# Performance work log

Measured on AMD Instinct MI355X. Metric: run time of the kernel, lower is better.

## Reference

```python
import jax, jax.numpy as jnp
import numpy as np

NUM_INPUTS = 512
NUM_OUTPUTS = 256
NUM_NODES = 20000
NUM_EDGES = 640000
NUM_LAYERS = 6
BATCH = 128


def setup_inputs() -> dict:
    rng = np.random.default_rng(0)
    chunk = (NUM_NODES - NUM_INPUTS) // NUM_LAYERS  # 3248 nodes per topo layer
    # destination node of each edge: any non-input node
    dst = rng.integers(NUM_INPUTS, NUM_INPUTS + chunk * NUM_LAYERS, NUM_EDGES)
    layer_of = (dst - NUM_INPUTS) // chunk
    layer_start = NUM_INPUTS + layer_of * chunk  # first node index of dst's layer
    # source strictly in an earlier layer (or an input node) -> layered DAG
    src = (rng.random(NUM_EDGES) * layer_start).astype(np.int64)
    act_id = rng.integers(0, 3, NUM_NODES)  # 0=sigmoid, 1=tanh, 2=relu
    layer_masks = np.zeros((NUM_LAYERS, NUM_NODES), dtype=bool)
    for l in range(NUM_LAYERS):
        layer_masks[l, NUM_INPUTS + l * chunk: NUM_INPUTS + (l + 1) * chunk] = True
    key = jax.random.key(0)
    kx, kw = jax.random.split(key)
    x = jax.random.normal(kx, (BATCH, NUM_INPUTS), dtype=jnp.float32)
    weights = jax.random.normal(kw, (NUM_EDGES,), dtype=jnp.float32) * 0.05
    return {
        "x": x,
        "weights": weights,
        "edge_src": jnp.asarray(src, dtype=jnp.int64),
        "edge_dst": jnp.asarray(dst, dtype=jnp.int64),
        "act_id": jnp.asarray(act_id, dtype=jnp.int64),
        "layer_masks": jnp.asarray(layer_masks),
        "steps": 1,
    }


def reference(x, weights, edge_src, edge_dst, act_id, layer_masks, steps):
    # Non-recurrent sparse path of NeatModule.forward (steps == 1).
    B = x.shape[0]
    N = layer_masks.shape[1]
    # state[:, input_nodes] = x ; all other nodes start at 0
    state = jnp.zeros((B, N), dtype=x.dtype).at[:, : x.shape[1]].set(x)
    is_sig = (act_id == 0)[None, :]
    is_tanh = (act_id == 1)[None, :]
    for l in range(layer_masks.shape[0]):  # loop over topological layers (fixed, small)
        # total_input = W^T @ state  (sparse mm), expressed as gather + segment_sum
        msgs = state.T[edge_src] * weights[:, None]                    # [E, B]
        tot = jax.ops.segment_sum(msgs, edge_dst, num_segments=N).T   # [B, N]
        act = jnp.where(is_sig, jax.nn.sigmoid(tot),
                        jnp.where(is_tanh, jnp.tanh(tot), jax.nn.relu(tot)))
        # only nodes of this layer get updated
        state = jnp.where(layer_masks[l][None, :], act, state)
    return state[:, -NUM_OUTPUTS:]
```

## Files before the change

### kernel.cpp

```cpp
#include <hip/hip_runtime.h>
#include <hip/hip_bf16.h>

#define N_IN     512
#define N_OUTS   256
#define N_NODES  20000
#define N_EDGES  640000
#define N_LAYERS 6
#define BATCH    128
#define CHUNK    3248

#define NPART    8
#define PART_SZ  2500
#define SCAT_NB  104

#define CSR_LOG2 7
#define CSR_STRIDE (1 << CSR_LOG2)

typedef unsigned int   uint32;
typedef unsigned short ushort16;

static constexpr size_t OFF_STATE = 0;
static constexpr size_t OFF_CNT   = (size_t)N_NODES * BATCH * 2;
static constexpr size_t OFF_CSR   = OFF_CNT + (size_t)N_NODES * 4;

__device__ __forceinline__ float bf16bits_to_f32(uint32 bits) {
    union { uint32 u; float f; } c; c.u = bits << 16; return c.f;
}
__device__ __forceinline__ ushort16 f32_to_bf16bits(float f) {
    union { float f; uint32 u; } c; c.f = f;
    uint32 lsb = (c.u >> 16) & 1u;
    c.u += 0x7FFFu + lsb;
    return (ushort16)(c.u >> 16);
}

__device__ __forceinline__ int detect_f32_wave(const ushort16* __restrict__ p) {
    int lane = threadIdx.x & 63;
    int ex = (p[lane] >> 7) & 0xFF;
    return __any(ex >= 134) ? 1 : 0;
}
__device__ __forceinline__ bool detect_i64(const int* __restrict__ dst32) {
    return dst32[1] == 0;
}

__device__ __forceinline__ float act_apply(int a, float x) {
    if (a == 0) return 1.f / (1.f + __expf(-x));
    if (a == 1) return tanhf(x);
    return fmaxf(x, 0.f);
}

__global__ void k_init(const ushort16* __restrict__ xb,
                       ushort16* __restrict__ state,
                       int* __restrict__ cnt) {
    const int f32 = detect_f32_wave(xb);
    const int idx = blockIdx.x * 256 + threadIdx.x;
    int n = idx >> 7, b = idx & 127;
    ushort16 v;
    if (f32) v = f32_to_bf16bits(((const float*)xb)[b * N_IN + n]);
    else     v = xb[b * N_IN + n];
    state[idx] = v;
    if (idx < N_NODES) cnt[idx] = 0;
}

__global__ void k_scatter(const int* __restrict__ src32,
                          const int* __restrict__ dst32,
                          const ushort16* __restrict__ wraw,
                          int* __restrict__ cnt,
                          uint32* __restrict__ csr) {
    const int f32  = detect_f32_wave(wraw);
    const int part = blockIdx.x & (NPART - 1);
    const int slice = blockIdx.x >> 3;
    const int nthr = (gridDim.x >> 3) * 256;
    const int tid0 = slice * 256 + threadIdx.x;
    if (detect_i64(dst32)) {
        const int4* d4 = (const int4*)dst32;
        const int4* s4 = (const int4*)src32;
        for (int p = tid0; p < N_EDGES / 2; p += nthr) {
            int4 dq = d4[p];
            int d0 = dq.x, d1 = dq.z;
            bool m0 = (d0 / PART_SZ) == part, m1 = (d1 / PART_SZ) == part;
            if (!m0 && !m1) continue;
            int4 sq = s4[p];
            uint32 w0b, w1b;
            if (f32) {
                float2 wf = ((const float2*)wraw)[p];
                w0b = f32_to_bf16bits(wf.x); w1b = f32_to_bf16bits(wf.y);
            } else {
                uint32 wb = ((const uint32*)wraw)[p];
                w0b = wb & 0xFFFFu; w1b = wb >> 16;
            }
            if (m0) {
                int pos = atomicAdd(&cnt[d0], 1);
                if (pos < CSR_STRIDE) csr[((size_t)d0 << CSR_LOG2) + pos] = ((uint32)sq.x << 16) | w0b;
            }
            if (m1) {
                int pos = atomicAdd(&cnt[d1], 1);
                if (pos < CSR_STRIDE) csr[((size_t)d1 << CSR_LOG2) + pos] = ((uint32)sq.z << 16) | w1b;
            }
        }
    } else {
        const int4* d4 = (const int4*)dst32;
        const int4* s4 = (const int4*)src32;
        for (int p = tid0; p < N_EDGES / 4; p += nthr) {
            int4 dq = d4[p];
            bool m0 = (dq.x / PART_SZ) == part, m1 = (dq.y / PART_SZ) == part;
            bool m2 = (dq.z / PART_SZ) == part, m3 = (dq.w / PART_SZ) == part;
            if (!(m0 | m1 | m2 | m3)) continue;
            int4 sq = s4[p];
            uint32 wb0, wb1, wb2, wb3;
            if (f32) {
                float4 wf = ((const float4*)wraw)[p];
                wb0 = f32_to_bf16bits(wf.x); wb1 = f32_to_bf16bits(wf.y);
                wb2 = f32_to_bf16bits(wf.z); wb3 = f32_to_bf16bits(wf.w);
            } else {
                uint2 wu = ((const uint2*)wraw)[p];
                wb0 = wu.x & 0xFFFFu; wb1 = wu.x >> 16;
                wb2 = wu.y & 0xFFFFu; wb3 = wu.y >> 16;
            }
            if (m0) { int pos = atomicAdd(&cnt[dq.x], 1);
                      if (pos < CSR_STRIDE) csr[((size_t)dq.x << CSR_LOG2) + pos] = ((uint32)sq.x << 16) | wb0; }
            if (m1) { int pos = atomicAdd(&cnt[dq.y], 1);
                      if (pos < CSR_STRIDE) csr[((size_t)dq.y << CSR_LOG2) + pos] = ((uint32)sq.y << 16) | wb1; }
            if (m2) { int pos = atomicAdd(&cnt[dq.z], 1);
                      if (pos < CSR_STRIDE) csr[((size_t)dq.z << CSR_LOG2) + pos] = ((uint32)sq.z << 16) | wb2; }
            if (m3) { int pos = atomicAdd(&cnt[dq.w], 1);
                      if (pos < CSR_STRIDE) csr[((size_t)dq.w << CSR_LOG2) + pos] = ((uint32)sq.w << 16) | wb3; }
        }
    }
}

__global__ void __launch_bounds__(BATCH)
k_layer(ushort16* __restrict__ state,
        const int* __restrict__ cnt,
        const uint32* __restrict__ csr,
        const int* __restrict__ act32,
        const int* __restrict__ dst32,
        int base) {
    const int node = base + blockIdx.x;
    const int b = threadIdx.x;
    const int lo = node << CSR_LOG2;
    const int hi = lo + cnt[node];
    float acc = 0.f;
    int e = lo;
    for (; e + 8 <= hi; e += 8) {
        uint32 p0 = csr[e],     p1 = csr[e + 1];
        uint32 p2 = csr[e + 2], p3 = csr[e + 3];
        uint32 p4 = csr[e + 4], p5 = csr[e + 5];
        uint32 p6 = csr[e + 6], p7 = csr[e + 7];
        float v0 = bf16bits_to_f32(state[(size_t)(p0 >> 16) * BATCH + b]);
        float v1 = bf16bits_to_f32(state[(size_t)(p1 >> 16) * BATCH + b]);
        float v2 = bf16bits_to_f32(state[(size_t)(p2 >> 16) * BATCH + b]);
        float v3 = bf16bits_to_f32(state[(size_t)(p3 >> 16) * BATCH + b]);
        float v4 = bf16bits_to_f32(state[(size_t)(p4 >> 16) * BATCH + b]);
        float v5 = bf16bits_to_f32(state[(size_t)(p5 >> 16) * BATCH + b]);
        float v6 = bf16bits_to_f32(state[(size_t)(p6 >> 16) * BATCH + b]);
        float v7 = bf16bits_to_f32(state[(size_t)(p7 >> 16) * BATCH + b]);
        acc = fmaf(bf16bits_to_f32(p0 & 0xFFFFu), v0, acc);
        acc = fmaf(bf16bits_to_f32(p1 & 0xFFFFu), v1, acc);
        acc = fmaf(bf16bits_to_f32(p2 & 0xFFFFu), v2, acc);
        acc = fmaf(bf16bits_to_f32(p3 & 0xFFFFu), v3, acc);
        acc = fmaf(bf16bits_to_f32(p4 & 0xFFFFu), v4, acc);
        acc = fmaf(bf16bits_to_f32(p5 & 0xFFFFu), v5, acc);
        acc = fmaf(bf16bits_to_f32(p6 & 0xFFFFu), v6, acc);
        acc = fmaf(bf16bits_to_f32(p7 & 0xFFFFu), v7, acc);
    }
    for (; e < hi; ++e) {
        uint32 p = csr[e];
        float v = bf16bits_to_f32(state[(size_t)(p >> 16) * BATCH + b]);
        acc = fmaf(bf16bits_to_f32(p & 0xFFFFu), v, acc);
    }
    const int istride = detect_i64(dst32) ? 2 : 1;
    const int a = act32[(size_t)node * istride];
    state[(size_t)node * BATCH + b] = f32_to_bf16bits(act_apply(a, acc));
}

__global__ void k_out(const ushort16* __restrict__ state,
                      const ushort16* __restrict__ xb,
                      void* __restrict__ out) {
    const int f32 = detect_f32_wave(xb);
    int idx = blockIdx.x * 256 + threadIdx.x;
    int b = idx >> 8, j = idx & 255;
    ushort16 v = state[(size_t)(N_NODES - N_OUTS + j) * BATCH + b];
    if (f32) ((float*)out)[idx] = bf16bits_to_f32(v);
    else     ((ushort16*)out)[idx] = v;
}

extern "C" void kernel_launch(void* const* d_in, const int* in_sizes, int n_in,
                              void* d_out, int out_size, void* d_ws, size_t ws_size,
                              hipStream_t stream) {
    const ushort16* x_raw = (const ushort16*)d_in[0];
    const ushort16* w_raw = (const ushort16*)d_in[1];
    const int* src32 = (const int*)d_in[2];
    const int* dst32 = (const int*)d_in[3];
    const int* act32 = (const int*)d_in[4];
    (void)d_in[5]; (void)d_in[6]; (void)in_sizes; (void)n_in; (void)out_size; (void)ws_size;

    char* ws = (char*)d_ws;
    ushort16* state = (ushort16*)(ws + OFF_STATE);
    int*    cnt = (int*)(ws + OFF_CNT);
    uint32* csr = (uint32*)(ws + OFF_CSR);

    k_init<<<(N_IN * BATCH) / 256, 256, 0, stream>>>(x_raw, state, cnt);
    k_scatter<<<NPART * SCAT_NB, 256, 0, stream>>>(src32, dst32, w_raw, cnt, csr);

    for (int l = 0; l < N_LAYERS; ++l) {
        int base = N_IN + l * CHUNK;
        k_layer<<<CHUNK, BATCH, 0, stream>>>(state, cnt, csr, act32, dst32, base);
    }

    k_out<<<(BATCH * N_OUTS) / 256, 256, 0, stream>>>(state, x_raw, d_out);
}
```

Measured before the change: 88.37 us.

## Compute only output nodes in last layer and fuse init into scatter

The last topological layer now computes only the 256 output nodes and writes them directly to the output, skipping the other last-layer nodes that are never read. Their edges are also dropped during CSR construction. The input-state init is folded into the scatter kernel, the counter reset becomes a memset, and the gather loop is unrolled to 16. The skipped work is truly dead for this computation, but it relies on the fixed layer layout constants, including the hardcoded L5_START.

```diff
diff --git a/kernel.cpp b/kernel.cpp
--- a/kernel.cpp
+++ b/kernel.cpp
@@ -8,6 +8,8 @@
 #define N_LAYERS 6
 #define BATCH    128
 #define CHUNK    3248
+#define L5_START 16752
+#define OUT_BASE (N_NODES - N_OUTS)
 
 #define NPART    8
 #define PART_SZ  2500
@@ -48,25 +50,27 @@
     return fmaxf(x, 0.f);
 }
 
-__global__ void k_init(const ushort16* __restrict__ xb,
-                       ushort16* __restrict__ state,
-                       int* __restrict__ cnt) {
-    const int f32 = detect_f32_wave(xb);
-    const int idx = blockIdx.x * 256 + threadIdx.x;
-    int n = idx >> 7, b = idx & 127;
-    ushort16 v;
-    if (f32) v = f32_to_bf16bits(((const float*)xb)[b * N_IN + n]);
-    else     v = xb[b * N_IN + n];
-    state[idx] = v;
-    if (idx < N_NODES) cnt[idx] = 0;
-}
-
-__global__ void k_scatter(const int* __restrict__ src32,
+__device__ __forceinline__ bool is_dead(int d) {
+    return d >= L5_START && d < OUT_BASE;
+}
+
+__global__ void k_scatter(const ushort16* __restrict__ xb,
+                          const int* __restrict__ src32,
                           const int* __restrict__ dst32,
                           const ushort16* __restrict__ wraw,
+                          ushort16* __restrict__ state,
                           int* __restrict__ cnt,
                           uint32* __restrict__ csr) {
-    const int f32  = detect_f32_wave(wraw);
+    const int f32x = detect_f32_wave(xb);
+    const int f32w = detect_f32_wave(wraw);
+    {
+        const int idx = blockIdx.x * 256 + threadIdx.x;
+        if (idx < N_IN * BATCH) {
+            int n = idx >> 7, b = idx & 127;
+            state[idx] = f32x ? f32_to_bf16bits(((const float*)xb)[b * N_IN + n])
+                              : xb[b * N_IN + n];
+        }
+    }
     const int part = blockIdx.x & (NPART - 1);
     const int slice = blockIdx.x >> 3;
     const int nthr = (gridDim.x >> 3) * 256;
@@ -77,11 +81,12 @@
         for (int p = tid0; p < N_EDGES / 2; p += nthr) {
             int4 dq = d4[p];
             int d0 = dq.x, d1 = dq.z;
-            bool m0 = (d0 / PART_SZ) == part, m1 = (d1 / PART_SZ) == part;
+            bool m0 = (d0 / PART_SZ) == part && !is_dead(d0);
+            bool m1 = (d1 / PART_SZ) == part && !is_dead(d1);
             if (!m0 && !m1) continue;
             int4 sq = s4[p];
             uint32 w0b, w1b;
-            if (f32) {
+            if (f32w) {
                 float2 wf = ((const float2*)wraw)[p];
                 w0b = f32_to_bf16bits(wf.x); w1b = f32_to_bf16bits(wf.y);
             } else {
@@ -102,12 +107,14 @@
         const int4* s4 = (const int4*)src32;
         for (int p = tid0; p < N_EDGES / 4; p += nthr) {
             int4 dq = d4[p];
-            bool m0 = (dq.x / PART_SZ) == part, m1 = (dq.y / PART_SZ) == part;
-            bool m2 = (dq.z / PART_SZ) == part, m3 = (dq.w / PART_SZ) == part;
+            bool m0 = (dq.x / PART_SZ) == part && !is_dead(dq.x);
+            bool m1 = (dq.y / PART_SZ) == part && !is_dead(dq.y);
+            bool m2 = (dq.z / PART_SZ) == part && !is_dead(dq.z);
+            bool m3 = (dq.w / PART_SZ) == part && !is_dead(dq.w);
             if (!(m0 | m1 | m2 | m3)) continue;
             int4 sq = s4[p];
             uint32 wb0, wb1, wb2, wb3;
-            if (f32) {
+            if (f32w) {
                 float4 wf = ((const float4*)wraw)[p];
                 wb0 = f32_to_bf16bits(wf.x); wb1 = f32_to_bf16bits(wf.y);
                 wb2 = f32_to_bf16bits(wf.z); wb3 = f32_to_bf16bits(wf.w);
@@ -128,6 +135,44 @@
     }
 }
 
+__device__ __forceinline__ float gather_acc(int node, int b,
+                                            const ushort16* __restrict__ state,
+                                            const int* __restrict__ cnt,
+                                            const uint32* __restrict__ csr) {
+    const int lo = node << CSR_LOG2;
+    const int hi = lo + cnt[node];
+    float acc = 0.f;
+    int e = lo;
+    for (; e + 16 <= hi; e += 16) {
+        uint32 p[16]; float v[16];
+#pragma unroll
+        for (int k = 0; k < 16; ++k) p[k] = csr[e + k];
+#pragma unroll
+        for (int k = 0; k < 16; ++k)
+            v[k] = bf16bits_to_f32(state[(size_t)(p[k] >> 16) * BATCH + b]);
+#pragma unroll
+        for (int k = 0; k < 16; ++k)
+            acc = fmaf(bf16bits_to_f32(p[k] & 0xFFFFu), v[k], acc);
+    }
+    for (; e + 4 <= hi; e += 4) {
+        uint32 p[4]; float v[4];
+#pragma unroll
+        for (int k = 0; k < 4; ++k) p[k] = csr[e + k];
+#pragma unroll
+        for (int k = 0; k < 4; ++k)
+            v[k] = bf16bits_to_f32(state[(size_t)(p[k] >> 16) * BATCH + b]);
+#pragma unroll
+        for (int k = 0; k < 4; ++k)
+            acc = fmaf(bf16bits_to_f32(p[k] & 0xFFFFu), v[k], acc);
+    }
+    for (; e < hi; ++e) {
+        uint32 p = csr[e];
+        float v = bf16bits_to_f32(state[(size_t)(p >> 16) * BATCH + b]);
+        acc = fmaf(bf16bits_to_f32(p & 0xFFFFu), v, acc);
+    }
+    return acc;
+}
+
 __global__ void __launch_bounds__(BATCH)
 k_layer(ushort16* __restrict__ state,
         const int* __restrict__ cnt,
@@ -137,51 +182,31 @@
         int base) {
     const int node = base + blockIdx.x;
     const int b = threadIdx.x;
-    const int lo = node << CSR_LOG2;
-    const int hi = lo + cnt[node];
-    float acc = 0.f;
-    int e = lo;
-    for (; e + 8 <= hi; e += 8) {
-        uint32 p0 = csr[e],     p1 = csr[e + 1];
-        uint32 p2 = csr[e + 2], p3 = csr[e + 3];
-        uint32 p4 = csr[e + 4], p5 = csr[e + 5];
-        uint32 p6 = csr[e + 6], p7 = csr[e + 7];
-        float v0 = bf16bits_to_f32(state[(size_t)(p0 >> 16) * BATCH + b]);
-        float v1 = bf16bits_to_f32(state[(size_t)(p1 >> 16) * BATCH + b]);
-        float v2 = bf16bits_to_f32(state[(size_t)(p2 >> 16) * BATCH + b]);
-        float v3 = bf16bits_to_f32(state[(size_t)(p3 >> 16) * BATCH + b]);
-        float v4 = bf16bits_to_f32(state[(size_t)(p4 >> 16) * BATCH + b]);
-        float v5 = bf16bits_to_f32(state[(size_t)(p5 >> 16) * BATCH + b]);
-        float v6 = bf16bits_to_f32(state[(size_t)(p6 >> 16) * BATCH + b]);
-        float v7 = bf16bits_to_f32(state[(size_t)(p7 >> 16) * BATCH + b]);
-        acc = fmaf(bf16bits_to_f32(p0 & 0xFFFFu), v0, acc);
-        acc = fmaf(bf16bits_to_f32(p1 & 0xFFFFu), v1, acc);
-        acc = fmaf(bf16bits_to_f32(p2 & 0xFFFFu), v2, acc);
-        acc = fmaf(bf16bits_to_f32(p3 & 0xFFFFu), v3, acc);
-        acc = fmaf(bf16bits_to_f32(p4 & 0xFFFFu), v4, acc);
-        acc = fmaf(bf16bits_to_f32(p5 & 0xFFFFu), v5, acc);
-        acc = fmaf(bf16bits_to_f32(p6 & 0xFFFFu), v6, acc);
-        acc = fmaf(bf16bits_to_f32(p7 & 0xFFFFu), v7, acc);
-    }
-    for (; e < hi; ++e) {
-        uint32 p = csr[e];
-        float v = bf16bits_to_f32(state[(size_t)(p >> 16) * BATCH + b]);
-        acc = fmaf(bf16bits_to_f32(p & 0xFFFFu), v, acc);
-    }
+    float acc = gather_acc(node, b, state, cnt, csr);
     const int istride = detect_i64(dst32) ? 2 : 1;
     const int a = act32[(size_t)node * istride];
     state[(size_t)node * BATCH + b] = f32_to_bf16bits(act_apply(a, acc));
 }
 
-__global__ void k_out(const ushort16* __restrict__ state,
-                      const ushort16* __restrict__ xb,
-                      void* __restrict__ out) {
-    const int f32 = detect_f32_wave(xb);
-    int idx = blockIdx.x * 256 + threadIdx.x;
-    int b = idx >> 8, j = idx & 255;
-    ushort16 v = state[(size_t)(N_NODES - N_OUTS + j) * BATCH + b];
-    if (f32) ((float*)out)[idx] = bf16bits_to_f32(v);
-    else     ((ushort16*)out)[idx] = v;
+__global__ void __launch_bounds__(BATCH)
+k_out_layer(const ushort16* __restrict__ state,
+            const int* __restrict__ cnt,
+            const uint32* __restrict__ csr,
+            const int* __restrict__ act32,
+            const int* __restrict__ dst32,
+            const ushort16* __restrict__ xb,
+            void* __restrict__ out) {
+    const int f32x = detect_f32_wave(xb);
+    const int j = blockIdx.x;
+    const int node = OUT_BASE + j;
+    const int b = threadIdx.x;
+    float acc = gather_acc(node, b, state, cnt, csr);
+    const int istride = detect_i64(dst32) ? 2 : 1;
+    const int a = act32[(size_t)node * istride];
+    float r = act_apply(a, acc);
+    ushort16 rb = f32_to_bf16bits(r);
+    if (f32x) ((float*)out)[(b << 8) | j] = bf16bits_to_f32(rb);
+    else      ((ushort16*)out)[(b << 8) | j] = rb;
 }
 
 extern "C" void kernel_launch(void* const* d_in, const int* in_sizes, int n_in,
@@ -199,13 +224,16 @@
     int*    cnt = (int*)(ws + OFF_CNT);
     uint32* csr = (uint32*)(ws + OFF_CSR);
 
-    k_init<<<(N_IN * BATCH) / 256, 256, 0, stream>>>(x_raw, state, cnt);
-    k_scatter<<<NPART * SCAT_NB, 256, 0, stream>>>(src32, dst32, w_raw, cnt, csr);
-
-    for (int l = 0; l < N_LAYERS; ++l) {
+    hipMemsetAsync(cnt, 0, (size_t)N_NODES * 4, stream);
+
+    k_scatter<<<NPART * SCAT_NB, 256, 0, stream>>>(x_raw, src32, dst32, w_raw,
+                                                    state, cnt, csr);
+
+    for (int l = 0; l < N_LAYERS - 1; ++l) {
         int base = N_IN + l * CHUNK;
         k_layer<<<CHUNK, BATCH, 0, stream>>>(state, cnt, csr, act32, dst32, base);
     }
 
-    k_out<<<(BATCH * N_OUTS) / 256, 256, 0, stream>>>(state, x_raw, d_out);
-}
+    k_out_layer<<<N_OUTS, BATCH, 0, stream>>>(state, cnt, csr, act32, dst32,
+                                              x_raw, d_out);
+}
```

Result: faster. 80.42 us (-9.0%).
